# Optimization experiments

Hardware: AMD Instinct MI355X
Metric: run time of the kernel (lower is better)

Reference implementation:

```python
import jax, jax.numpy as jnp
import numpy as np

L_LAYERS = 4
N_HEADS = 8
TAU = 1.0

def _gelu(x):
    return jax.nn.gelu(x, approximate=False)

def _ln(x, g, b, eps=1e-5):
    m = jnp.mean(x, axis=-1, keepdims=True)
    v = jnp.var(x, axis=-1, keepdims=True)
    return (x - m) * jax.lax.rsqrt(v + eps) * g + b

def _attn(x, Wq, bq, Wk, bk, Wv, bv, Wo, bo):
    B, N, D = x.shape
    H = N_HEADS
    Dh = D // H
    q = (x @ Wq + bq).reshape(B, N, H, Dh)
    k = (x @ Wk + bk).reshape(B, N, H, Dh)
    v = (x @ Wv + bv).reshape(B, N, H, Dh)
    scores = jnp.einsum('bnhd,bmhd->bhnm', q, k) / jnp.sqrt(jnp.asarray(Dh, x.dtype))
    a = jax.nn.softmax(scores, axis=-1)
    o = jnp.einsum('bhnm,bmhd->bnhd', a, v).reshape(B, N, D)
    return o @ Wo + bo


def setup_inputs() -> dict:
    B, N, D, DFF, E, HID = 64, 128, 512, 2048, 32, 64
    L = L_LAYERS
    key = jax.random.key(0)
    ks = iter(jax.random.split(key, 64))
    def nrm(shape, s):
        return jax.random.normal(next(ks), shape, jnp.float32) * jnp.float32(s)
    s_d = 1.0 / np.sqrt(D)
    inp = {}
    inp['base_samples'] = jax.random.normal(next(ks), (B, N), jnp.float32)
    inp['int_samples'] = jax.random.normal(next(ks), (B, N), jnp.float32)
    inp['target_row'] = jax.random.normal(next(ks), (B, N), jnp.float32)
    inp['int_mask'] = (jax.random.uniform(next(ks), (B, N)) < 0.5).astype(jnp.float32)
    inp['int_node_idx'] = jax.random.randint(next(ks), (B,), 0, N)
    # Gumbel(0,1) noise: -log(Exp(1)) matches -empty.exponential_().log()
    inp['g_noise'] = -jnp.log(jax.random.exponential(next(ks), (B, N, N), jnp.float32))
    # encoder (Linear 4 -> D over stacked per-node scalars)
    inp['enc_W'] = nrm((4, D), 0.5)
    inp['enc_b'] = jnp.zeros((D,), jnp.float32)
    # transformer layers (stacked across L)
    inp['Wq'] = nrm((L, D, D), s_d); inp['bq'] = jnp.zeros((L, D), jnp.float32)
    inp['Wk'] = nrm((L, D, D), s_d); inp['bk'] = jnp.zeros((L, D), jnp.float32)
    inp['Wv'] = nrm((L, D, D), s_d); inp['bv'] = jnp.zeros((L, D), jnp.float32)
    inp['Wo'] = nrm((L, D, D), s_d); inp['bo'] = jnp.zeros((L, D), jnp.float32)
    inp['ln1_g'] = jnp.ones((L, D), jnp.float32); inp['ln1_b'] = jnp.zeros((L, D), jnp.float32)
    inp['W_ff1'] = nrm((L, D, DFF), s_d); inp['b_ff1'] = jnp.zeros((L, DFF), jnp.float32)
    inp['W_ff2'] = nrm((L, DFF, D), 1.0 / np.sqrt(DFF)); inp['b_ff2'] = jnp.zeros((L, D), jnp.float32)
    inp['ln2_g'] = jnp.ones((L, D), jnp.float32); inp['ln2_b'] = jnp.zeros((L, D), jnp.float32)
    # intervention embedding + hyper net (32 -> 64 -> D)
    inp['emb'] = nrm((N, E), 1.0)
    inp['hyp_W1'] = nrm((E, HID), 1.0 / np.sqrt(E)); inp['hyp_b1'] = jnp.zeros((HID,), jnp.float32)
    inp['hyp_W2'] = nrm((HID, D), 1.0 / np.sqrt(HID)); inp['hyp_b2'] = jnp.zeros((D,), jnp.float32)
    # per-node delta experts, stacked: Linear(D,D)-GELU-Linear(D,1)
    inp['exp_W1'] = nrm((N, D, D), s_d); inp['exp_b1'] = jnp.zeros((N, D), jnp.float32)
    inp['exp_W2'] = nrm((N, D), s_d); inp['exp_b2'] = jnp.zeros((N,), jnp.float32)
    # DAG heads
    inp['dagp_W'] = nrm((D, D), s_d); inp['dagp_b'] = jnp.zeros((D,), jnp.float32)
    inp['dagc_W'] = nrm((D, D), s_d); inp['dagc_b'] = jnp.zeros((D,), jnp.float32)
    return inp


def reference(base_samples, int_samples, target_row, int_mask, int_node_idx, g_noise,
              enc_W, enc_b, Wq, bq, Wk, bk, Wv, bv, Wo, bo, ln1_g, ln1_b,
              W_ff1, b_ff1, W_ff2, b_ff2, ln2_g, ln2_b, emb,
              hyp_W1, hyp_b1, hyp_W2, hyp_b2,
              exp_W1, exp_b1, exp_W2, exp_b2,
              dagp_W, dagp_b, dagc_W, dagc_b):
    # encoder: per-node scalar features -> d_model
    feats = jnp.stack([base_samples, int_samples, target_row, int_mask], axis=-1)  # [B,N,4]
    x = feats @ enc_W + enc_b  # [B,N,D]
    # post-norm transformer encoder (gelu FFN, eval-mode: no dropout)
    for l in range(L_LAYERS):
        x = _ln(x + _attn(x, Wq[l], bq[l], Wk[l], bk[l], Wv[l], bv[l], Wo[l], bo[l]),
                ln1_g[l], ln1_b[l])
        h = _gelu(x @ W_ff1[l] + b_ff1[l]) @ W_ff2[l] + b_ff2[l]
        x = _ln(x + h, ln2_g[l], ln2_b[l])
    # hyper-network modulation
    instr = emb[int_node_idx]  # [B,32]
    mod = _gelu(instr @ hyp_W1 + hyp_b1) @ hyp_W2 + hyp_b2  # [B,D]
    xm = x * mod[:, None, :]  # [B,N,D]
    # per-node experts fused into grouped batched GEMMs
    h = _gelu(jnp.einsum('bnd,nde->bne', xm, exp_W1) + exp_b1)  # [B,N,D]
    deltas = jnp.einsum('bnd,nd->bn', h, exp_W2) + exp_b2  # [B,N]
    # DAG logits + gumbel-sigmoid (soft, eval mode)
    p = x @ dagp_W + dagp_b
    c = x @ dagc_W + dagc_b
    logits = jnp.einsum('bnd,bmd->bnm', p, c)  # [B,N,N]
    adj_sampled = jax.nn.sigmoid((logits + g_noise) / TAU)
    return (deltas, logits, adj_sampled)
```

## Files before the change

### kernel.cpp

```cpp
#include <hip/hip_runtime.h>
#include <hip/hip_bf16.h>
#include <math.h>

#define BB 64
#define NN 128
#define DD 512
#define DFF 2048
#define HH 8
#define DHH 64
#define EE 32
#define HID 64
#define LL 4
#define NTOK (BB*NN)
#define LDQKV 1536

typedef __hip_bfloat16 bf16;
typedef __attribute__((ext_vector_type(8))) short short8v;
typedef __attribute__((ext_vector_type(4))) float f32x4v;

__device__ __forceinline__ float b2f(bf16 x) { return __bfloat162float(x); }
__device__ __forceinline__ bf16 f2b(float x) { return __float2bfloat16(x); }
__device__ __forceinline__ float gelu_f(float x) {
    return 0.5f * x * (1.0f + erff(x * 0.7071067811865476f));
}
__device__ __forceinline__ void glds16(const bf16* g, bf16* l) {
    __builtin_amdgcn_global_load_lds(
        (const __attribute__((address_space(1))) unsigned int*)g,
        (__attribute__((address_space(3))) unsigned int*)l,
        16, 0, 0);
}

union F4B8 { float4 f; bf16 h[8]; };
union B2U { bf16 h[2]; unsigned int u; };

__global__ __launch_bounds__(256) void transpose_prep(
    const float* __restrict__ in, bf16* __restrict__ out, int K, int N,
    long long sIn, long long sOut)
{
    __shared__ float t[32][33];
    int g = blockIdx.z;
    in  += (size_t)g * sIn;
    out += (size_t)g * sOut;
    int n0 = blockIdx.x * 32, k0 = blockIdx.y * 32;
    int tx = threadIdx.x & 31, ty = threadIdx.x >> 5;
#pragma unroll
    for (int i = 0; i < 32; i += 8)
        t[ty + i][tx] = in[(size_t)(k0 + ty + i) * N + n0 + tx];
    __syncthreads();
#pragma unroll
    for (int i = 0; i < 32; i += 8)
        out[(size_t)(n0 + ty + i) * K + k0 + tx] = f2b(t[tx][ty + i]);
}

__global__ __launch_bounds__(256) void pack_qkv_bias(
    const float* __restrict__ bq, const float* __restrict__ bk,
    const float* __restrict__ bv, float* __restrict__ o)
{
    int i = blockIdx.x * 256 + threadIdx.x;
    if (i >= LL * LDQKV) return;
    int l = i / LDQKV, j = i % LDQKV;
    float v = (j < 512) ? bq[l*512 + j]
            : (j < 1024 ? bk[l*512 + j - 512] : bv[l*512 + j - 1024]);
    o[i] = v;
}
__global__ __launch_bounds__(256) void pack_dag_bias(
    const float* __restrict__ dp, const float* __restrict__ dc, float* __restrict__ o)
{
    int i = blockIdx.x * 256 + threadIdx.x;
    if (i >= 1024) return;
    o[i] = (i < 512) ? dp[i] : dc[i - 512];
}

__global__ __launch_bounds__(256) void encoder_kernel(
    const float* __restrict__ bs, const float* __restrict__ ins,
    const float* __restrict__ tr, const float* __restrict__ im,
    const float* __restrict__ encW, const float* __restrict__ encB,
    bf16* __restrict__ X)
{
    int idx = blockIdx.x * 256 + threadIdx.x;
    size_t i8 = (size_t)idx * 8;
    int d0 = (int)(i8 & (DD - 1));
    int t  = (int)(i8 >> 9);
    float f0 = bs[t], f1 = ins[t], f2 = tr[t], f3 = im[t];
    alignas(16) float acc[8], w[8];
    *(float4*)&acc[0] = *(const float4*)&encB[d0];
    *(float4*)&acc[4] = *(const float4*)&encB[d0 + 4];
    const float fs[4] = {f0, f1, f2, f3};
#pragma unroll
    for (int k = 0; k < 4; k++) {
        *(float4*)&w[0] = *(const float4*)&encW[k * DD + d0];
        *(float4*)&w[4] = *(const float4*)&encW[k * DD + d0 + 4];
#pragma unroll
        for (int j = 0; j < 8; j++) acc[j] = fmaf(fs[k], w[j], acc[j]);
    }
    F4B8 o;
#pragma unroll
    for (int j = 0; j < 8; j++) o.h[j] = f2b(acc[j]);
    *(float4*)&X[i8] = o.f;
}

template<int BM,int BN,int WM,int WN,int ACT,bool TRANSB,bool HAS_BIAS,
         typename TB,typename TC>
__global__ __launch_bounds__(WM*WN*64) void gemm2(
    const bf16* __restrict__ A, const TB* __restrict__ Bw,
    const float* __restrict__ bias, TC* __restrict__ C,
    int K, int lda, int ldb, int ldc,
    long long sAg, long long sBg, long long sbg, long long sCg)
{
    constexpr int BK = 64;
    constexpr int NT = WM*WN*64;
    constexpr int NW = NT/64;
    constexpr int MI = BM/WM/16;
    constexpr int NI = BN/WN/16;
    constexpr int LDK = TRANSB ? BK : (BK + 8);
    constexpr int LDC = BN + 8;
    constexpr size_t SH_AB = (size_t)2*(BM+BN)*LDK*sizeof(bf16);
    constexpr size_t SH_C  = (size_t)BM*LDC*sizeof(TC);
    __shared__ __align__(16) char smem[(SH_AB > SH_C ? SH_AB : SH_C)];
    bf16* AsB = (bf16*)smem;
    bf16* BsB = AsB + (size_t)2*BM*LDK;
    TC*   Cs  = (TC*)smem;

    const int g = blockIdx.z;
    const bf16* Ag = A + (size_t)g * sAg;
    const TB*   Bg = Bw + (size_t)g * sBg;

    int bx = blockIdx.x, by = blockIdx.y;
    if (gridDim.z == 1) {
        int nwg = gridDim.x * gridDim.y;
        if ((nwg & 7) == 0) {
            int id = by * gridDim.x + bx;
            id = (id & 7) * (nwg >> 3) + (id >> 3);
            bx = id % gridDim.x;
            by = id / gridDim.x;
        }
    }
    const int m0 = by * BM, n0 = bx * BN;
    const int tid = threadIdx.x, lane = tid & 63, wid = tid >> 6;
    const int wm = wid / WN, wn = wid % WN;
    const int lr = lane & 15, lq = lane >> 4;
    const int KT = K / BK;

    f32x4v acc[MI][NI];
#pragma unroll
    for (int mi = 0; mi < MI; mi++)
#pragma unroll
        for (int ni = 0; ni < NI; ni++)
            acc[mi][ni] = (f32x4v){0.f, 0.f, 0.f, 0.f};

    if constexpr (TRANSB) {
        auto stage = [&](int kt, int p) {
#pragma unroll
            for (int q = wid; q < BM/8; q += NW) {
                int r = q*8 + (lane >> 3), sp = lane & 7;
                glds16(Ag + (size_t)(m0 + r)*lda + kt*BK + ((sp ^ (r & 7)) << 3),
                       AsB + ((size_t)p*BM + q*8)*BK);
            }
#pragma unroll
            for (int q = wid; q < BN/8; q += NW) {
                int r = q*8 + (lane >> 3), sp = lane & 7;
                glds16((const bf16*)Bg + (size_t)(n0 + r)*ldb + kt*BK + ((sp ^ (r & 7)) << 3),
                       BsB + ((size_t)p*BN + q*8)*BK);
            }
        };
        stage(0, 0);
        __syncthreads();
        const int rx7 = lr & 7;
        int p = 0;
        for (int kt = 0; kt < KT; ++kt) {
            if (kt + 1 < KT) stage(kt + 1, p ^ 1);
#pragma unroll
            for (int kk = 0; kk < 2; ++kk) {
                const int colo = ((((kk << 2) | lq) ^ rx7) << 3);
                short8v av[MI], bv[NI];
#pragma unroll
                for (int mi = 0; mi < MI; ++mi) {
                    int row = wm*(BM/WM) + mi*16 + lr;
                    av[mi] = *(const short8v*)&AsB[((size_t)p*BM + row)*BK + colo];
                }
#pragma unroll
                for (int ni = 0; ni < NI; ++ni) {
                    int row = wn*(BN/WN) + ni*16 + lr;
                    bv[ni] = *(const short8v*)&BsB[((size_t)p*BN + row)*BK + colo];
                }
#pragma unroll
                for (int mi = 0; mi < MI; ++mi)
#pragma unroll
                    for (int ni = 0; ni < NI; ++ni)
                        acc[mi][ni] = __builtin_amdgcn_mfma_f32_16x16x32_bf16(
                            av[mi], bv[ni], acc[mi][ni], 0, 0, 0);
            }
            __syncthreads();
            p ^= 1;
        }
    } else {
        constexpr int RA  = (BM*(BK/8))/NT;
        constexpr int RBF = (BK*(BN/4))/NT;
        float4 rA[RA];
        float4 rF[RBF];
        auto issue = [&](int kt) {
#pragma unroll
            for (int r = 0; r < RA; ++r) {
                int c = tid + r*NT; int row = c >> 3, k8 = (c & 7) << 3;
                rA[r] = *(const float4*)(Ag + (size_t)(m0+row)*lda + kt*BK + k8);
            }
#pragma unroll
            for (int r = 0; r < RBF; ++r) {
                int c = tid + r*NT; int kk = c/(BN/4), n4 = (c%(BN/4))*4;
                rF[r] = *(const float4*)((const float*)Bg + (size_t)(kt*BK+kk)*ldb + n0 + n4);
            }
        };
        auto commit = [&](int p) {
#pragma unroll
            for (int r = 0; r < RA; ++r) {
                int c = tid + r*NT; int row = c >> 3, k8 = (c & 7) << 3;
                *(float4*)&AsB[((size_t)p*BM + row)*LDK + k8] = rA[r];
            }
#pragma unroll
            for (int r = 0; r < RBF; ++r) {
                int c = tid + r*NT; int kk = c/(BN/4), n4 = (c%(BN/4))*4;
                int kg = kk >> 3, kw = kk & 7;
                alignas(16) float vv[4]; *(float4*)vv = rF[r];
#pragma unroll
                for (int i = 0; i < 4; ++i) {
                    int n = n4 + i;
                    AsB[0] = AsB[0];
                    BsB[((size_t)p*BN + n)*LDK + (((kg ^ ((n>>2)&7)) << 3) | kw)] = f2b(vv[i]);
                }
            }
        };
        issue(0); commit(0); __syncthreads();
        for (int kt = 0; kt < KT; ++kt) {
            if (kt + 1 < KT) issue(kt + 1);
            const int p = kt & 1;
#pragma unroll
            for (int kk = 0; kk < 2; ++kk) {
                short8v av[MI], bv[NI];
#pragma unroll
                for (int mi = 0; mi < MI; ++mi) {
                    int row = wm*(BM/WM) + mi*16 + lr;
                    av[mi] = *(const short8v*)&AsB[((size_t)p*BM + row)*LDK + kk*32 + lq*8];
                }
#pragma unroll
                for (int ni = 0; ni < NI; ++ni) {
                    int row = wn*(BN/WN) + ni*16 + lr;
                    int col = (((kk*4 + lq) ^ ((row>>2)&7)) << 3);
                    bv[ni] = *(const short8v*)&BsB[((size_t)p*BN + row)*LDK + col];
                }
#pragma unroll
                for (int mi = 0; mi < MI; ++mi)
#pragma unroll
                    for (int ni = 0; ni < NI; ++ni)
                        acc[mi][ni] = __builtin_amdgcn_mfma_f32_16x16x32_bf16(
                            av[mi], bv[ni], acc[mi][ni], 0, 0, 0);
            }
            if (kt + 1 < KT) { commit((kt + 1) & 1); }
            __syncthreads();
        }
    }
    __syncthreads();

#pragma unroll
    for (int mi = 0; mi < MI; ++mi) {
        int rb = wm*(BM/WM) + mi*16 + lq*4;
#pragma unroll
        for (int ni = 0; ni < NI; ++ni) {
            int cc = wn*(BN/WN) + ni*16 + lr;
            float bvv = 0.f;
            if constexpr (HAS_BIAS) bvv = bias[(size_t)g*sbg + n0 + cc];
#pragma unroll
            for (int r = 0; r < 4; ++r) {
                float v = acc[mi][ni][r] + bvv;
                if (ACT == 1) v = gelu_f(v);
                if constexpr (sizeof(TC) == 2) Cs[(rb+r)*LDC + cc] = (TC)f2b(v);
                else ((float*)Cs)[(rb+r)*LDC + cc] = v;
            }
        }
    }
    __syncthreads();

    TC* Cg = C + (size_t)g * sCg;
    constexpr int VEC = 16 / sizeof(TC);
#pragma unroll
    for (int c = tid; c < BM*(BN/VEC); c += NT) {
        int row = c / (BN/VEC), col = (c % (BN/VEC)) * VEC;
        *(float4*)&Cg[(size_t)(m0+row)*ldc + n0 + col] = *(const float4*)&Cs[row*LDC + col];
    }
}

__global__ __launch_bounds__(256) void attn_mfma(bf16* __restrict__ QKV)
{
    __shared__ bf16 Ps[NN][NN + 8];
    __shared__ bf16 Vt[DHH][NN + 8];
    int bh = blockIdx.x;
    int h = bh & (HH - 1);
    int b = bh >> 3;
    const int tid = threadIdx.x;
    const int lane = tid & 63;
    const int w = tid >> 6;
    const int lr = lane & 15;
    const int lq = lane >> 4;
    const size_t baseQ = (size_t)(b * NN) * LDQKV + h * DHH;
    const size_t baseK = baseQ + 512;
    const size_t baseV = baseQ + 1024;

    for (int c = tid; c < 512; c += 256) {
        int m = (c >> 3) * 2;
        int d8 = (c & 7) * 8;
        F4B8 v0, v1;
        v0.f = *(const float4*)(QKV + baseV + (size_t)m * LDQKV + d8);
        v1.f = *(const float4*)(QKV + baseV + (size_t)(m + 1) * LDQKV + d8);
#pragma unroll
        for (int j = 0; j < 8; j++) {
            B2U pk; pk.h[0] = v0.h[j]; pk.h[1] = v1.h[j];
            *(unsigned int*)&Vt[d8 + j][m] = pk.u;
        }
    }

    f32x4v sacc[2][8];
#pragma unroll
    for (int mi = 0; mi < 2; mi++)
#pragma unroll
        for (int ni = 0; ni < 8; ni++)
            sacc[mi][ni] = (f32x4v){0.f, 0.f, 0.f, 0.f};
#pragma unroll
    for (int ks = 0; ks < 2; ks++) {
        short8v aq[2];
#pragma unroll
        for (int mi = 0; mi < 2; mi++) {
            int row = w * 32 + mi * 16 + lr;
            aq[mi] = *(const short8v*)(QKV + baseQ + (size_t)row * LDQKV + ks * 32 + lq * 8);
        }
#pragma unroll
        for (int ni = 0; ni < 8; ni++) {
            int col = ni * 16 + lr;
            short8v bk = *(const short8v*)(QKV + baseK + (size_t)col * LDQKV + ks * 32 + lq * 8);
#pragma unroll
            for (int mi = 0; mi < 2; mi++)
                sacc[mi][ni] = __builtin_amdgcn_mfma_f32_16x16x32_bf16(
                    aq[mi], bk, sacc[mi][ni], 0, 0, 0);
        }
    }

#pragma unroll
    for (int mi = 0; mi < 2; mi++) {
#pragma unroll
        for (int r = 0; r < 4; r++) {
            float mx = -1e30f;
#pragma unroll
            for (int ni = 0; ni < 8; ni++)
                mx = fmaxf(mx, sacc[mi][ni][r]);
            mx = fmaxf(mx, __shfl_xor(mx, 1, 64));
            mx = fmaxf(mx, __shfl_xor(mx, 2, 64));
            mx = fmaxf(mx, __shfl_xor(mx, 4, 64));
            mx = fmaxf(mx, __shfl_xor(mx, 8, 64));
            mx *= 0.125f;
            float s = 0.f;
#pragma unroll
            for (int ni = 0; ni < 8; ni++) {
                float e = __expf(sacc[mi][ni][r] * 0.125f - mx);
                sacc[mi][ni][r] = e; s += e;
            }
            s += __shfl_xor(s, 1, 64);
            s += __shfl_xor(s, 2, 64);
            s += __shfl_xor(s, 4, 64);
            s += __shfl_xor(s, 8, 64);
            float inv = 1.0f / s;
            int row = w * 32 + mi * 16 + lq * 4 + r;
#pragma unroll
            for (int ni = 0; ni < 8; ni++)
                Ps[row][ni * 16 + lr] = f2b(sacc[mi][ni][r] * inv);
        }
    }
    __syncthreads();

    f32x4v oacc[2][4];
#pragma unroll
    for (int mi = 0; mi < 2; mi++)
#pragma unroll
        for (int ni = 0; ni < 4; ni++)
            oacc[mi][ni] = (f32x4v){0.f, 0.f, 0.f, 0.f};
#pragma unroll
    for (int ks = 0; ks < 4; ks++) {
        short8v ap[2];
#pragma unroll
        for (int mi = 0; mi < 2; mi++)
            ap[mi] = *(const short8v*)&Ps[w * 32 + mi * 16 + lr][ks * 32 + lq * 8];
#pragma unroll
        for (int ni = 0; ni < 4; ni++) {
            short8v bv = *(const short8v*)&Vt[ni * 16 + lr][ks * 32 + lq * 8];
#pragma unroll
            for (int mi = 0; mi < 2; mi++)
                oacc[mi][ni] = __builtin_amdgcn_mfma_f32_16x16x32_bf16(
                    ap[mi], bv, oacc[mi][ni], 0, 0, 0);
        }
    }
    __syncthreads();
#pragma unroll
    for (int mi = 0; mi < 2; mi++)
#pragma unroll
        for (int ni = 0; ni < 4; ni++) {
            int d = ni * 16 + lr;
#pragma unroll
            for (int r = 0; r < 4; r++) {
                int row = w * 32 + mi * 16 + lq * 4 + r;
                Ps[row][d] = f2b(oacc[mi][ni][r]);
            }
        }
    __syncthreads();
    for (int c = tid; c < NN * (DHH/8); c += 256) {
        int row = c >> 3, d8 = (c & 7) * 8;
        *(float4*)(QKV + baseQ + (size_t)row * LDQKV + d8) = *(const float4*)&Ps[row][d8];
    }
}

__global__ __launch_bounds__(256) void add_ln_kernel(
    bf16* __restrict__ X, const bf16* __restrict__ R, int ldr,
    const float* __restrict__ g, const float* __restrict__ bt)
{
    int tok = blockIdx.x * 4 + (threadIdx.x >> 6);
    int lane = threadIdx.x & 63;
    size_t base = (size_t)tok * DD + lane * 8;
    size_t rbase = (size_t)tok * ldr + lane * 8;
    F4B8 x, r;
    x.f = *(const float4*)&X[base];
    r.f = *(const float4*)&R[rbase];
    float v[8]; float s = 0.f, s2 = 0.f;
#pragma unroll
    for (int j = 0; j < 8; j++) {
        v[j] = b2f(x.h[j]) + b2f(r.h[j]);
        s += v[j]; s2 += v[j] * v[j];
    }
#pragma unroll
    for (int m = 1; m < 64; m <<= 1) {
        s  += __shfl_xor(s, m, 64);
        s2 += __shfl_xor(s2, m, 64);
    }
    float mean = s * (1.0f / 512.0f);
    float var = fmaxf(s2 * (1.0f / 512.0f) - mean * mean, 0.0f);
    float rstd = rsqrtf(var + 1e-5f);
    alignas(16) float gv[8], bv[8];
    *(float4*)&gv[0] = *(const float4*)&g[lane * 8];
    *(float4*)&gv[4] = *(const float4*)&g[lane * 8 + 4];
    *(float4*)&bv[0] = *(const float4*)&bt[lane * 8];
    *(float4*)&bv[4] = *(const float4*)&bt[lane * 8 + 4];
    F4B8 o;
#pragma unroll
    for (int j = 0; j < 8; j++)
        o.h[j] = f2b((v[j] - mean) * rstd * gv[j] + bv[j]);
    *(float4*)&X[base] = o.f;
}

__global__ __launch_bounds__(512) void hyper_kernel(
    const int* __restrict__ idx, const float* __restrict__ emb,
    const float* __restrict__ W1, const float* __restrict__ b1,
    const float* __restrict__ W2, const float* __restrict__ b2,
    float* __restrict__ MODp)
{
    int b = blockIdx.x;
    int t = threadIdx.x;
    __shared__ float instr[EE];
    __shared__ float h1[HID];
    int id = idx[b];
    if (t < EE) instr[t] = emb[id*EE + t];
    __syncthreads();
    if (t < HID) {
        float a = b1[t];
        for (int i = 0; i < EE; i++) a += instr[i] * W1[i*HID + t];
        h1[t] = gelu_f(a);
    }
    __syncthreads();
    float a = b2[t];
    for (int i = 0; i < HID; i++) a += h1[i] * W2[i*DD + t];
    MODp[(size_t)b*DD + t] = a;
}

__global__ __launch_bounds__(256) void xm_kernel(
    const bf16* __restrict__ X, const float* __restrict__ MODp,
    bf16* __restrict__ XM)
{
    int idx = blockIdx.x * 256 + threadIdx.x;
    size_t i8 = (size_t)idx * 8;
    int b = (int)(i8 >> 16);
    int d0 = (int)(i8 & (DD - 1));
    F4B8 x; x.f = *(const float4*)&X[i8];
    alignas(16) float mv[8];
    *(float4*)&mv[0] = *(const float4*)&MODp[b * DD + d0];
    *(float4*)&mv[4] = *(const float4*)&MODp[b * DD + d0 + 4];
    F4B8 o;
#pragma unroll
    for (int j = 0; j < 8; j++) o.h[j] = f2b(b2f(x.h[j]) * mv[j]);
    *(float4*)&XM[i8] = o.f;
}

__global__ __launch_bounds__(256) void deltas_kernel(
    const bf16* __restrict__ HE, const float* __restrict__ W2,
    const float* __restrict__ b2, float* __restrict__ out)
{
    int rid = blockIdx.x * 4 + (threadIdx.x >> 6);
    int lane = threadIdx.x & 63;
    int n = rid >> 6;
    int b = rid & 63;
    const bf16* hrow = HE + ((size_t)n * BB + b) * DD + lane * 8;
    const float* wrow = W2 + (size_t)n * DD + lane * 8;
    F4B8 hv; hv.f = *(const float4*)hrow;
    alignas(16) float wv[8];
    *(float4*)&wv[0] = *(const float4*)&wrow[0];
    *(float4*)&wv[4] = *(const float4*)&wrow[4];
    float s = 0.f;
#pragma unroll
    for (int j = 0; j < 8; j++) s += b2f(hv.h[j]) * wv[j];
#pragma unroll
    for (int m = 1; m < 64; m <<= 1) s += __shfl_xor(s, m, 64);
    if (lane == 0) out[b * NN + n] = s + b2[n];
}

__global__ __launch_bounds__(256) void finalize_kernel(
    const float* __restrict__ lg, const float* __restrict__ gn,
    float* __restrict__ out_adj)
{
    int idx = blockIdx.x * 256 + threadIdx.x;
    size_t i4 = (size_t)idx * 4;
    float4 l = *(const float4*)&lg[i4];
    float4 n = *(const float4*)&gn[i4];
    float4 o;
    o.x = 1.0f / (1.0f + __expf(-(l.x + n.x)));
    o.y = 1.0f / (1.0f + __expf(-(l.y + n.y)));
    o.z = 1.0f / (1.0f + __expf(-(l.z + n.z)));
    o.w = 1.0f / (1.0f + __expf(-(l.w + n.w)));
    *(float4*)&out_adj[i4] = o;
}

template<int BM,int BN,int WM,int WN,int ACT,bool HB,typename TC>
static inline void launch2(bool useT, dim3 grid, hipStream_t s,
    const bf16* A, const float* Wf, const bf16* Wt, const float* bias, TC* C,
    int K, int lda, int ldbF, int ldbT, int ldc,
    long long sAg, long long sBg, long long sbg, long long sCg)
{
    if (useT)
        gemm2<BM,BN,WM,WN,ACT,true ,HB,bf16 ,TC><<<grid,WM*WN*64,0,s>>>(
            A, Wt, bias, C, K, lda, ldbT, ldc, sAg,sBg,sbg,sCg);
    else
        gemm2<BM,BN,WM,WN,ACT,false,HB,float,TC><<<grid,WM*WN*64,0,s>>>(
            A, Wf, bias, C, K, lda, ldbF, ldc, sAg,sBg,sbg,sCg);
}

extern "C" void kernel_launch(void* const* d_in, const int* in_sizes, int n_in,
                              void* d_out, int out_size, void* d_ws, size_t ws_size,
                              hipStream_t stream)
{
    const float* base_s = (const float*)d_in[0];
    const float* int_s  = (const float*)d_in[1];
    const float* targ   = (const float*)d_in[2];
    const float* maskv  = (const float*)d_in[3];
    const int*   nidx   = (const int*)  d_in[4];
    const float* gnoise = (const float*)d_in[5];
    const float* encW = (const float*)d_in[6];
    const float* encB = (const float*)d_in[7];
    const float* Wq = (const float*)d_in[8];  const float* bq = (const float*)d_in[9];
    const float* Wk = (const float*)d_in[10]; const float* bk = (const float*)d_in[11];
    const float* Wv = (const float*)d_in[12]; const float* bv = (const float*)d_in[13];
    const float* Wo = (const float*)d_in[14]; const float* bo = (const float*)d_in[15];
    const float* ln1g = (const float*)d_in[16]; const float* ln1b = (const float*)d_in[17];
    const float* Wff1 = (const float*)d_in[18]; const float* bff1 = (const float*)d_in[19];
    const float* Wff2 = (const float*)d_in[20]; const float* bff2 = (const float*)d_in[21];
    const float* ln2g = (const float*)d_in[22]; const float* ln2b = (const float*)d_in[23];
    const float* emb  = (const float*)d_in[24];
    const float* hW1 = (const float*)d_in[25]; const float* hb1 = (const float*)d_in[26];
    const float* hW2 = (const float*)d_in[27]; const float* hb2 = (const float*)d_in[28];
    const float* eW1 = (const float*)d_in[29]; const float* eb1 = (const float*)d_in[30];
    const float* eW2 = (const float*)d_in[31]; const float* eb2 = (const float*)d_in[32];
    const float* dpW = (const float*)d_in[33]; const float* dpB = (const float*)d_in[34];
    const float* dcW = (const float*)d_in[35]; const float* dcB = (const float*)d_in[36];

    float* out_deltas = (float*)d_out;
    float* out_logits = out_deltas + (size_t)BB*NN;
    float* out_adj    = out_logits + (size_t)BB*NN*NN;

    const size_t SZ = (size_t)NTOK * DD;

    const size_t WT_ELEMS = (size_t)3*LL*DD*DD + (size_t)LL*DD*DD
                          + 2*(size_t)LL*DD*DFF + 2*(size_t)DD*DD;
    const size_t NEED_BIG = 6*SZ*2 + (size_t)BB*DD*4;
    const size_t NEED_P0  = NEED_BIG + WT_ELEMS*2 + (LL*LDQKV + 1024)*4;
    const bool big = ws_size >= NEED_BIG;
    const bool p0  = ws_size >= NEED_P0;

    bf16* X  = (bf16*)d_ws;
    bf16* PK = X + SZ;
    bf16* F2 = PK + 4*SZ;
    float* MODp = big ? (float*)(F2 + SZ) : (float*)(PK + 3*SZ);

    bf16 *wqkvT=nullptr,*woT=nullptr,*wf1T=nullptr,*wf2T=nullptr,*dagT=nullptr;
    float *qkvB=nullptr,*dagB=nullptr;
    if (p0) {
        bf16* WT = (bf16*)(MODp + (size_t)BB*DD);
        wqkvT = WT;
        woT   = wqkvT + (size_t)3*LL*DD*DD;
        wf1T  = woT + (size_t)LL*DD*DD;
        wf2T  = wf1T + (size_t)LL*DD*DFF;
        dagT  = wf2T + (size_t)LL*DD*DFF;
        qkvB  = (float*)(dagT + 2*(size_t)DD*DD);
        dagB  = qkvB + LL*LDQKV;

        transpose_prep<<<dim3(16,16,LL),256,0,stream>>>(Wq, wqkvT,           DD, DD, (long long)DD*DD, (long long)LDQKV*DD);
        transpose_prep<<<dim3(16,16,LL),256,0,stream>>>(Wk, wqkvT+512*512,   DD, DD, (long long)DD*DD, (long long)LDQKV*DD);
        transpose_prep<<<dim3(16,16,LL),256,0,stream>>>(Wv, wqkvT+1024*512,  DD, DD, (long long)DD*DD, (long long)LDQKV*DD);
        transpose_prep<<<dim3(16,16,LL),256,0,stream>>>(Wo, woT,             DD, DD, (long long)DD*DD, (long long)DD*DD);
        transpose_prep<<<dim3(64,16,LL),256,0,stream>>>(Wff1, wf1T,          DD, DFF,(long long)DD*DFF,(long long)DD*DFF);
        transpose_prep<<<dim3(16,64,LL),256,0,stream>>>(Wff2, wf2T,          DFF,DD, (long long)DD*DFF,(long long)DD*DFF);
        transpose_prep<<<dim3(16,16,1), 256,0,stream>>>(dpW, dagT,           DD, DD, 0, 0);
        transpose_prep<<<dim3(16,16,1), 256,0,stream>>>(dcW, dagT+512*512,   DD, DD, 0, 0);
        pack_qkv_bias<<<(LL*LDQKV+255)/256,256,0,stream>>>(bq, bk, bv, qkvB);
        pack_dag_bias<<<4,256,0,stream>>>(dpB, dcB, dagB);
    }

    encoder_kernel<<<NTOK*DD/8/256, 256, 0, stream>>>(
        base_s, int_s, targ, maskv, encW, encB, X);

    for (int l = 0; l < LL; ++l) {
        const size_t od = (size_t)l*DD*DD, of1 = (size_t)l*DD*DFF;
        if (p0) {
            gemm2<128,128,2,4,0,true,true,bf16,bf16><<<dim3(12,64,1),512,0,stream>>>(
                X, wqkvT + (size_t)l*LDQKV*DD, qkvB + (size_t)l*LDQKV, PK,
                DD, DD, DD, LDQKV, 0,0,0,0);
        } else {
            gemm2<128,128,2,4,0,false,true,float,bf16><<<dim3(4,64,1),512,0,stream>>>(
                X, Wq+od, bq+(size_t)l*DD, PK,        DD, DD, DD, LDQKV, 0,0,0,0);
            gemm2<128,128,2,4,0,false,true,float,bf16><<<dim3(4,64,1),512,0,stream>>>(
                X, Wk+od, bk+(size_t)l*DD, PK+512,    DD, DD, DD, LDQKV, 0,0,0,0);
            gemm2<128,128,2,4,0,false,true,float,bf16><<<dim3(4,64,1),512,0,stream>>>(
                X, Wv+od, bv+(size_t)l*DD, PK+1024,   DD, DD, DD, LDQKV, 0,0,0,0);
        }
        attn_mfma<<<BB*HH, 256, 0, stream>>>(PK);
        launch2<128,128,2,4,0,true,bf16>(p0, dim3(4,64,1), stream,
            PK, Wo+od, woT+od, bo+(size_t)l*DD, PK+512, DD, LDQKV, DD, DD, LDQKV, 0,0,0,0);
        add_ln_kernel<<<NTOK/4, 256, 0, stream>>>(X, PK+512, LDQKV,
            ln1g+(size_t)l*DD, ln1b+(size_t)l*DD);

        if (big) {
            launch2<128,128,2,4,1,true,bf16>(p0, dim3(16,64,1), stream,
                X, Wff1+of1, wf1T+of1, bff1+(size_t)l*DFF, PK,
                DD, DD, DFF, DD, DFF, 0,0,0,0);
            launch2<128,128,2,4,0,true,bf16>(p0, dim3(4,64,1), stream,
                PK, Wff2+of1, wf2T+of1, bff2+(size_t)l*DD, F2,
                DFF, DFF, DD, DFF, DD, 0,0,0,0);
            add_ln_kernel<<<NTOK/4, 256, 0, stream>>>(X, F2, DD,
                ln2g+(size_t)l*DD, ln2b+(size_t)l*DD);
        } else {
            for (int c = 0; c < 4; ++c) {
                launch2<128,128,2,4,1,true,bf16>(p0, dim3(16,16,1), stream,
                    X + (size_t)c*2048*DD, Wff1+of1, wf1T+of1, bff1+(size_t)l*DFF, PK,
                    DD, DD, DFF, DD, DFF, 0,0,0,0);
                launch2<128,128,2,4,0,true,bf16>(p0, dim3(4,16,1), stream,
                    PK, Wff2+of1, wf2T+of1, bff2+(size_t)l*DD, PK + 2*SZ + (size_t)c*2048*DD,
                    DFF, DFF, DD, DFF, DD, 0,0,0,0);
            }
            add_ln_kernel<<<NTOK/4, 256, 0, stream>>>(X, PK + 2*SZ, DD,
                ln2g+(size_t)l*DD, ln2b+(size_t)l*DD);
        }
    }

    hyper_kernel<<<BB, 512, 0, stream>>>(nidx, emb, hW1, hb1, hW2, hb2, MODp);
    bf16* XMb = big ? F2 : PK;
    xm_kernel<<<NTOK*DD/8/256, 256, 0, stream>>>(X, MODp, XMb);

    bf16* HEb = big ? PK : PK + SZ;
    gemm2<64,128,2,2,1,false,true,float,bf16><<<dim3(4,1,NN),256,0,stream>>>(
        XMb, eW1, eb1, HEb, DD, NN*DD, DD, DD,
        DD, (long long)DD*DD, DD, (long long)BB*DD);
    deltas_kernel<<<NN*BB/4, 256, 0, stream>>>(HEb, eW2, eb2, out_deltas);

    bf16* DAGb = PK;
    if (p0) {
        gemm2<128,128,2,4,0,true,true,bf16,bf16><<<dim3(8,64,1),512,0,stream>>>(
            X, dagT, dagB, DAGb, DD, DD, DD, 1024, 0,0,0,0);
    } else {
        gemm2<128,128,2,4,0,false,true,float,bf16><<<dim3(4,64,1),512,0,stream>>>(
            X, dpW, dpB, DAGb,       DD, DD, DD, 1024, 0,0,0,0);
        gemm2<128,128,2,4,0,false,true,float,bf16><<<dim3(4,64,1),512,0,stream>>>(
            X, dcW, dcB, DAGb + 512, DD, DD, DD, 1024, 0,0,0,0);
    }
    gemm2<64,64,2,2,0,true,false,bf16,float><<<dim3(2,2,BB),256,0,stream>>>(
        DAGb, DAGb + 512, (const float*)nullptr, out_logits,
        DD, 1024, 1024, NN,
        (long long)NN*1024, (long long)NN*1024, 0, (long long)NN*NN);
    finalize_kernel<<<BB*NN*NN/4/256, 256, 0, stream>>>(
        out_logits, gnoise, out_adj);

    (void)in_sizes; (void)n_in; (void)out_size;
}
```

Before: 598.9 us.

## Fuse modulation into expert GEMM, sigmoid into logits GEMM, batch prep launches

Merges the eight weight-transpose launches into one job-table kernel and the two bias-pack kernels into one. Folds the hypernetwork modulation multiply into the A-tile staging of the per-node expert GEMM, removing the separate xm pass and its intermediate buffer. Fuses the gumbel-sigmoid finalize into the logits GEMM epilogue so the logits are not read back from memory, and drops a dummy shared-memory store in the fp32-B commit loop. The trade-off is extra modulation loads inside the expert GEMM staging loop and more template variants.

```diff
diff --git a/kernel.cpp b/kernel.cpp
--- a/kernel.cpp
+++ b/kernel.cpp
@@ -33,15 +33,30 @@
 union F4B8 { float4 f; bf16 h[8]; };
 union B2U { bf16 h[2]; unsigned int u; };
 
-__global__ __launch_bounds__(256) void transpose_prep(
-    const float* __restrict__ in, bf16* __restrict__ out, int K, int N,
-    long long sIn, long long sOut)
+#define NJOBS 8
+struct TXJobs {
+    const float* in[NJOBS];
+    bf16* out[NJOBS];
+    int K[NJOBS], N[NJOBS];
+    long long sIn[NJOBS], sOut[NJOBS];
+    int tileEnd[NJOBS];
+};
+__global__ __launch_bounds__(256) void transpose_all(TXJobs jobs)
 {
     __shared__ float t[32][33];
-    int g = blockIdx.z;
-    in  += (size_t)g * sIn;
-    out += (size_t)g * sOut;
-    int n0 = blockIdx.x * 32, k0 = blockIdx.y * 32;
+    int tile = blockIdx.x;
+    int j = 0;
+    while (j < NJOBS - 1 && tile >= jobs.tileEnd[j]) ++j;
+    int base = j ? jobs.tileEnd[j-1] : 0;
+    int local = tile - base;
+    const int K = jobs.K[j], N = jobs.N[j];
+    const int tpg = (K >> 5) * (N >> 5);
+    int g  = local / tpg;
+    int r  = local % tpg;
+    int tX = r % (N >> 5), tY = r / (N >> 5);
+    const float* in = jobs.in[j] + (size_t)g * jobs.sIn[j];
+    bf16* out = jobs.out[j] + (size_t)g * jobs.sOut[j];
+    int n0 = tX * 32, k0 = tY * 32;
     int tx = threadIdx.x & 31, ty = threadIdx.x >> 5;
 #pragma unroll
     for (int i = 0; i < 32; i += 8)
@@ -52,23 +67,22 @@
         out[(size_t)(n0 + ty + i) * K + k0 + tx] = f2b(t[tx][ty + i]);
 }
 
-__global__ __launch_bounds__(256) void pack_qkv_bias(
+__global__ __launch_bounds__(256) void pack_bias(
     const float* __restrict__ bq, const float* __restrict__ bk,
-    const float* __restrict__ bv, float* __restrict__ o)
+    const float* __restrict__ bv, const float* __restrict__ dp,
+    const float* __restrict__ dc, float* __restrict__ qkvB,
+    float* __restrict__ dagB)
 {
     int i = blockIdx.x * 256 + threadIdx.x;
-    if (i >= LL * LDQKV) return;
-    int l = i / LDQKV, j = i % LDQKV;
-    float v = (j < 512) ? bq[l*512 + j]
-            : (j < 1024 ? bk[l*512 + j - 512] : bv[l*512 + j - 1024]);
-    o[i] = v;
-}
-__global__ __launch_bounds__(256) void pack_dag_bias(
-    const float* __restrict__ dp, const float* __restrict__ dc, float* __restrict__ o)
-{
-    int i = blockIdx.x * 256 + threadIdx.x;
-    if (i >= 1024) return;
-    o[i] = (i < 512) ? dp[i] : dc[i - 512];
+    if (i < LL * LDQKV) {
+        int l = i / LDQKV, j = i % LDQKV;
+        float v = (j < 512) ? bq[l*512 + j]
+                : (j < 1024 ? bk[l*512 + j - 512] : bv[l*512 + j - 1024]);
+        qkvB[i] = v;
+    } else if (i < LL * LDQKV + 1024) {
+        int j = i - LL * LDQKV;
+        dagB[j] = (j < 512) ? dp[j] : dc[j - 512];
+    }
 }
 
 __global__ __launch_bounds__(256) void encoder_kernel(
@@ -100,12 +114,14 @@
 }
 
 template<int BM,int BN,int WM,int WN,int ACT,bool TRANSB,bool HAS_BIAS,
-         typename TB,typename TC>
+         bool ASCALE,bool FUSE_ADJ,typename TB,typename TC>
 __global__ __launch_bounds__(WM*WN*64) void gemm2(
     const bf16* __restrict__ A, const TB* __restrict__ Bw,
     const float* __restrict__ bias, TC* __restrict__ C,
     int K, int lda, int ldb, int ldc,
-    long long sAg, long long sBg, long long sbg, long long sCg)
+    long long sAg, long long sBg, long long sbg, long long sCg,
+    const float* __restrict__ modp, const float* __restrict__ gn,
+    float* __restrict__ adjout)
 {
     constexpr int BK = 64;
     constexpr int NT = WM*WN*64;
@@ -198,7 +214,9 @@
         constexpr int RBF = (BK*(BN/4))/NT;
         float4 rA[RA];
         float4 rF[RBF];
+        int staged_kt = 0;
         auto issue = [&](int kt) {
+            staged_kt = kt;
 #pragma unroll
             for (int r = 0; r < RA; ++r) {
                 int c = tid + r*NT; int row = c >> 3, k8 = (c & 7) << 3;
@@ -214,7 +232,19 @@
 #pragma unroll
             for (int r = 0; r < RA; ++r) {
                 int c = tid + r*NT; int row = c >> 3, k8 = (c & 7) << 3;
-                *(float4*)&AsB[((size_t)p*BM + row)*LDK + k8] = rA[r];
+                if constexpr (ASCALE) {
+                    F4B8 u; u.f = rA[r];
+                    alignas(16) float m8[8];
+                    const float* mp = modp + (size_t)(m0+row)*DD + staged_kt*BK + k8;
+                    *(float4*)&m8[0] = *(const float4*)mp;
+                    *(float4*)&m8[4] = *(const float4*)(mp + 4);
+#pragma unroll
+                    for (int jj = 0; jj < 8; ++jj)
+                        u.h[jj] = f2b(b2f(u.h[jj]) * m8[jj]);
+                    *(float4*)&AsB[((size_t)p*BM + row)*LDK + k8] = u.f;
+                } else {
+                    *(float4*)&AsB[((size_t)p*BM + row)*LDK + k8] = rA[r];
+                }
             }
 #pragma unroll
             for (int r = 0; r < RBF; ++r) {
@@ -224,7 +254,6 @@
 #pragma unroll
                 for (int i = 0; i < 4; ++i) {
                     int n = n4 + i;
-                    AsB[0] = AsB[0];
                     BsB[((size_t)p*BN + n)*LDK + (((kg ^ ((n>>2)&7)) << 3) | kw)] = f2b(vv[i]);
                 }
             }
@@ -279,12 +308,22 @@
     }
     __syncthreads();
 
-    TC* Cg = C + (size_t)g * sCg;
     constexpr int VEC = 16 / sizeof(TC);
 #pragma unroll
     for (int c = tid; c < BM*(BN/VEC); c += NT) {
         int row = c / (BN/VEC), col = (c % (BN/VEC)) * VEC;
-        *(float4*)&Cg[(size_t)(m0+row)*ldc + n0 + col] = *(const float4*)&Cs[row*LDC + col];
+        size_t gidx = (size_t)g*sCg + (size_t)(m0+row)*ldc + n0 + col;
+        *(float4*)&C[gidx] = *(const float4*)&Cs[row*LDC + col];
+        if constexpr (FUSE_ADJ) {
+            float4 cv = *(const float4*)&Cs[row*LDC + col];
+            float4 g4 = *(const float4*)&gn[gidx];
+            float4 a4;
+            a4.x = 1.0f / (1.0f + __expf(-(cv.x + g4.x)));
+            a4.y = 1.0f / (1.0f + __expf(-(cv.y + g4.y)));
+            a4.z = 1.0f / (1.0f + __expf(-(cv.z + g4.z)));
+            a4.w = 1.0f / (1.0f + __expf(-(cv.w + g4.w)));
+            *(float4*)&adjout[gidx] = a4;
+        }
     }
 }
 
@@ -475,24 +514,6 @@
     MODp[(size_t)b*DD + t] = a;
 }
 
-__global__ __launch_bounds__(256) void xm_kernel(
-    const bf16* __restrict__ X, const float* __restrict__ MODp,
-    bf16* __restrict__ XM)
-{
-    int idx = blockIdx.x * 256 + threadIdx.x;
-    size_t i8 = (size_t)idx * 8;
-    int b = (int)(i8 >> 16);
-    int d0 = (int)(i8 & (DD - 1));
-    F4B8 x; x.f = *(const float4*)&X[i8];
-    alignas(16) float mv[8];
-    *(float4*)&mv[0] = *(const float4*)&MODp[b * DD + d0];
-    *(float4*)&mv[4] = *(const float4*)&MODp[b * DD + d0 + 4];
-    F4B8 o;
-#pragma unroll
-    for (int j = 0; j < 8; j++) o.h[j] = f2b(b2f(x.h[j]) * mv[j]);
-    *(float4*)&XM[i8] = o.f;
-}
-
 __global__ __launch_bounds__(256) void deltas_kernel(
     const bf16* __restrict__ HE, const float* __restrict__ W2,
     const float* __restrict__ b2, float* __restrict__ out)
@@ -515,22 +536,6 @@
     if (lane == 0) out[b * NN + n] = s + b2[n];
 }
 
-__global__ __launch_bounds__(256) void finalize_kernel(
-    const float* __restrict__ lg, const float* __restrict__ gn,
-    float* __restrict__ out_adj)
-{
-    int idx = blockIdx.x * 256 + threadIdx.x;
-    size_t i4 = (size_t)idx * 4;
-    float4 l = *(const float4*)&lg[i4];
-    float4 n = *(const float4*)&gn[i4];
-    float4 o;
-    o.x = 1.0f / (1.0f + __expf(-(l.x + n.x)));
-    o.y = 1.0f / (1.0f + __expf(-(l.y + n.y)));
-    o.z = 1.0f / (1.0f + __expf(-(l.z + n.z)));
-    o.w = 1.0f / (1.0f + __expf(-(l.w + n.w)));
-    *(float4*)&out_adj[i4] = o;
-}
-
 template<int BM,int BN,int WM,int WN,int ACT,bool HB,typename TC>
 static inline void launch2(bool useT, dim3 grid, hipStream_t s,
     const bf16* A, const float* Wf, const bf16* Wt, const float* bias, TC* C,
@@ -538,11 +543,13 @@
     long long sAg, long long sBg, long long sbg, long long sCg)
 {
     if (useT)
-        gemm2<BM,BN,WM,WN,ACT,true ,HB,bf16 ,TC><<<grid,WM*WN*64,0,s>>>(
-            A, Wt, bias, C, K, lda, ldbT, ldc, sAg,sBg,sbg,sCg);
+        gemm2<BM,BN,WM,WN,ACT,true ,HB,false,false,bf16 ,TC><<<grid,WM*WN*64,0,s>>>(
+            A, Wt, bias, C, K, lda, ldbT, ldc, sAg,sBg,sbg,sCg,
+            nullptr, nullptr, nullptr);
     else
-        gemm2<BM,BN,WM,WN,ACT,false,HB,float,TC><<<grid,WM*WN*64,0,s>>>(
-            A, Wf, bias, C, K, lda, ldbF, ldc, sAg,sBg,sbg,sCg);
+        gemm2<BM,BN,WM,WN,ACT,false,HB,false,false,float,TC><<<grid,WM*WN*64,0,s>>>(
+            A, Wf, bias, C, K, lda, ldbF, ldc, sAg,sBg,sbg,sCg,
+            nullptr, nullptr, nullptr);
 }
 
 extern "C" void kernel_launch(void* const* d_in, const int* in_sizes, int n_in,
@@ -603,16 +610,24 @@
         qkvB  = (float*)(dagT + 2*(size_t)DD*DD);
         dagB  = qkvB + LL*LDQKV;
 
-        transpose_prep<<<dim3(16,16,LL),256,0,stream>>>(Wq, wqkvT,           DD, DD, (long long)DD*DD, (long long)LDQKV*DD);
-        transpose_prep<<<dim3(16,16,LL),256,0,stream>>>(Wk, wqkvT+512*512,   DD, DD, (long long)DD*DD, (long long)LDQKV*DD);
-        transpose_prep<<<dim3(16,16,LL),256,0,stream>>>(Wv, wqkvT+1024*512,  DD, DD, (long long)DD*DD, (long long)LDQKV*DD);
-        transpose_prep<<<dim3(16,16,LL),256,0,stream>>>(Wo, woT,             DD, DD, (long long)DD*DD, (long long)DD*DD);
-        transpose_prep<<<dim3(64,16,LL),256,0,stream>>>(Wff1, wf1T,          DD, DFF,(long long)DD*DFF,(long long)DD*DFF);
-        transpose_prep<<<dim3(16,64,LL),256,0,stream>>>(Wff2, wf2T,          DFF,DD, (long long)DD*DFF,(long long)DD*DFF);
-        transpose_prep<<<dim3(16,16,1), 256,0,stream>>>(dpW, dagT,           DD, DD, 0, 0);
-        transpose_prep<<<dim3(16,16,1), 256,0,stream>>>(dcW, dagT+512*512,   DD, DD, 0, 0);
-        pack_qkv_bias<<<(LL*LDQKV+255)/256,256,0,stream>>>(bq, bk, bv, qkvB);
-        pack_dag_bias<<<4,256,0,stream>>>(dpB, dcB, dagB);
+        TXJobs J;
+        int acc = 0;
+        auto addjob = [&](int j, const float* in, bf16* out, int K, int N,
+                          long long sIn, long long sOut, int G) {
+            J.in[j]=in; J.out[j]=out; J.K[j]=K; J.N[j]=N; J.sIn[j]=sIn; J.sOut[j]=sOut;
+            acc += G * (K>>5) * (N>>5); J.tileEnd[j]=acc;
+        };
+        addjob(0, Wq,  wqkvT,          DD, DD, (long long)DD*DD, (long long)LDQKV*DD, LL);
+        addjob(1, Wk,  wqkvT+512*512,  DD, DD, (long long)DD*DD, (long long)LDQKV*DD, LL);
+        addjob(2, Wv,  wqkvT+1024*512, DD, DD, (long long)DD*DD, (long long)LDQKV*DD, LL);
+        addjob(3, Wo,  woT,            DD, DD, (long long)DD*DD, (long long)DD*DD,    LL);
+        addjob(4, Wff1,wf1T,           DD, DFF,(long long)DD*DFF,(long long)DD*DFF,   LL);
+        addjob(5, Wff2,wf2T,           DFF,DD, (long long)DD*DFF,(long long)DD*DFF,   LL);
+        addjob(6, dpW, dagT,           DD, DD, 0, 0, 1);
+        addjob(7, dcW, dagT+512*512,   DD, DD, 0, 0, 1);
+        transpose_all<<<acc, 256, 0, stream>>>(J);
+        pack_bias<<<(LL*LDQKV + 1024 + 255)/256, 256, 0, stream>>>(
+            bq, bk, bv, dpB, dcB, qkvB, dagB);
     }
 
     encoder_kernel<<<NTOK*DD/8/256, 256, 0, stream>>>(
@@ -621,16 +636,19 @@
     for (int l = 0; l < LL; ++l) {
         const size_t od = (size_t)l*DD*DD, of1 = (size_t)l*DD*DFF;
         if (p0) {
-            gemm2<128,128,2,4,0,true,true,bf16,bf16><<<dim3(12,64,1),512,0,stream>>>(
+            gemm2<128,128,2,4,0,true,true,false,false,bf16,bf16><<<dim3(12,64,1),512,0,stream>>>(
                 X, wqkvT + (size_t)l*LDQKV*DD, qkvB + (size_t)l*LDQKV, PK,
-                DD, DD, DD, LDQKV, 0,0,0,0);
+                DD, DD, DD, LDQKV, 0,0,0,0, nullptr, nullptr, nullptr);
         } else {
-            gemm2<128,128,2,4,0,false,true,float,bf16><<<dim3(4,64,1),512,0,stream>>>(
-                X, Wq+od, bq+(size_t)l*DD, PK,        DD, DD, DD, LDQKV, 0,0,0,0);
-            gemm2<128,128,2,4,0,false,true,float,bf16><<<dim3(4,64,1),512,0,stream>>>(
-                X, Wk+od, bk+(size_t)l*DD, PK+512,    DD, DD, DD, LDQKV, 0,0,0,0);
-            gemm2<128,128,2,4,0,false,true,float,bf16><<<dim3(4,64,1),512,0,stream>>>(
-                X, Wv+od, bv+(size_t)l*DD, PK+1024,   DD, DD, DD, LDQKV, 0,0,0,0);
+            gemm2<128,128,2,4,0,false,true,false,false,float,bf16><<<dim3(4,64,1),512,0,stream>>>(
+                X, Wq+od, bq+(size_t)l*DD, PK,        DD, DD, DD, LDQKV, 0,0,0,0,
+                nullptr, nullptr, nullptr);
+            gemm2<128,128,2,4,0,false,true,false,false,float,bf16><<<dim3(4,64,1),512,0,stream>>>(
+                X, Wk+od, bk+(size_t)l*DD, PK+512,    DD, DD, DD, LDQKV, 0,0,0,0,
+                nullptr, nullptr, nullptr);
+            gemm2<128,128,2,4,0,false,true,false,false,float,bf16><<<dim3(4,64,1),512,0,stream>>>(
+                X, Wv+od, bv+(size_t)l*DD, PK+1024,   DD, DD, DD, LDQKV, 0,0,0,0,
+                nullptr, nullptr, nullptr);
         }
         attn_mfma<<<BB*HH, 256, 0, stream>>>(PK);
         launch2<128,128,2,4,0,true,bf16>(p0, dim3(4,64,1), stream,
@@ -662,31 +680,28 @@
     }
 
     hyper_kernel<<<BB, 512, 0, stream>>>(nidx, emb, hW1, hb1, hW2, hb2, MODp);
-    bf16* XMb = big ? F2 : PK;
-    xm_kernel<<<NTOK*DD/8/256, 256, 0, stream>>>(X, MODp, XMb);
-
-    bf16* HEb = big ? PK : PK + SZ;
-    gemm2<64,128,2,2,1,false,true,float,bf16><<<dim3(4,1,NN),256,0,stream>>>(
-        XMb, eW1, eb1, HEb, DD, NN*DD, DD, DD,
-        DD, (long long)DD*DD, DD, (long long)BB*DD);
+
+    bf16* HEb = PK;
+    gemm2<64,128,2,2,1,false,true,true,false,float,bf16><<<dim3(4,1,NN),256,0,stream>>>(
+        X, eW1, eb1, HEb, DD, NN*DD, DD, DD,
+        DD, (long long)DD*DD, DD, (long long)BB*DD, MODp, nullptr, nullptr);
     deltas_kernel<<<NN*BB/4, 256, 0, stream>>>(HEb, eW2, eb2, out_deltas);
 
     bf16* DAGb = PK;
     if (p0) {
-        gemm2<128,128,2,4,0,true,true,bf16,bf16><<<dim3(8,64,1),512,0,stream>>>(
-            X, dagT, dagB, DAGb, DD, DD, DD, 1024, 0,0,0,0);
+        gemm2<128,128,2,4,0,true,true,false,false,bf16,bf16><<<dim3(8,64,1),512,0,stream>>>(
+            X, dagT, dagB, DAGb, DD, DD, DD, 1024, 0,0,0,0, nullptr, nullptr, nullptr);
     } else {
-        gemm2<128,128,2,4,0,false,true,float,bf16><<<dim3(4,64,1),512,0,stream>>>(
-            X, dpW, dpB, DAGb,       DD, DD, DD, 1024, 0,0,0,0);
-        gemm2<128,128,2,4,0,false,true,float,bf16><<<dim3(4,64,1),512,0,stream>>>(
-            X, dcW, dcB, DAGb + 512, DD, DD, DD, 1024, 0,0,0,0);
-    }
-    gemm2<64,64,2,2,0,true,false,bf16,float><<<dim3(2,2,BB),256,0,stream>>>(
+        gemm2<128,128,2,4,0,false,true,false,false,float,bf16><<<dim3(4,64,1),512,0,stream>>>(
+            X, dpW, dpB, DAGb,       DD, DD, DD, 1024, 0,0,0,0, nullptr, nullptr, nullptr);
+        gemm2<128,128,2,4,0,false,true,false,false,float,bf16><<<dim3(4,64,1),512,0,stream>>>(
+            X, dcW, dcB, DAGb + 512, DD, DD, DD, 1024, 0,0,0,0, nullptr, nullptr, nullptr);
+    }
+    gemm2<64,64,2,2,0,true,false,false,true,bf16,float><<<dim3(2,2,BB),256,0,stream>>>(
         DAGb, DAGb + 512, (const float*)nullptr, out_logits,
         DD, 1024, 1024, NN,
-        (long long)NN*1024, (long long)NN*1024, 0, (long long)NN*NN);
-    finalize_kernel<<<BB*NN*NN/4/256, 256, 0, stream>>>(
-        out_logits, gnoise, out_adj);
+        (long long)NN*1024, (long long)NN*1024, 0, (long long)NN*NN,
+        nullptr, gnoise, out_adj);
 
     (void)in_sizes; (void)n_in; (void)out_size;
 }
```

Result: faster. 568.7 us (-5.0%).
